# Optimization experiments

Measured on AMD Instinct MI355X. Metric: run time of the kernel, lower is better.

The kernel has to match this reference:

```python
import jax, jax.numpy as jnp
import numpy as np

E = 8        # num_adapters
K = 2        # top-k
DG = 1024    # extract_feature_size (gating input)
DI = 1024    # input_size (adapter input)
HG = 512     # gating hidden
H = 2048     # adapter hidden
C = 512      # adapter output (classes)
B = 4096     # batch
TEMP = 5.0   # gating softmax temperature
LOSS_COEF = 0.01
EPS = float(np.finfo(np.float64).eps)  # np.finfo(float).eps in combine()


def setup_inputs() -> dict:
    key = jax.random.key(0)
    ks = jax.random.split(key, 12)
    s = 0.02
    return {
        'x':   jax.random.normal(ks[0], (B, DG), jnp.float32),
        'x2':  jax.random.normal(ks[1], (B, DI), jnp.float32),
        'Wg1': jax.random.normal(ks[2], (DG, HG), jnp.float32) * s,
        'bg1': jnp.zeros((HG,), jnp.float32),
        'Wg2': jax.random.normal(ks[3], (HG, E), jnp.float32) * s,
        'bg2': jnp.zeros((E,), jnp.float32),
        'W1':  jax.random.normal(ks[4], (E, DI, H), jnp.float32) * s,
        'b1':  jnp.zeros((E, H), jnp.float32),
        'W2':  jax.random.normal(ks[5], (E, H, C), jnp.float32) * s,
        'b2':  jnp.zeros((E, C), jnp.float32),
    }


def _cv_squared(v):
    # torch .var() is unbiased (ddof=1)
    return v.var(ddof=1) / (v.mean() ** 2 + 1e-10)


def reference(x, x2, Wg1, bg1, Wg2, bg2, W1, b1, W2, b2):
    b = x.shape[0]
    # --- noisy_top_k_gating (eval path: no noise, dropout inactive) ---
    logits = jnp.maximum(x @ Wg1 + bg1, 0.0) @ Wg2 + bg2           # [B, E]
    top_vals, top_idx = jax.lax.top_k(logits, K)                   # [B, K]
    top_gates = jax.nn.softmax(top_vals / TEMP, axis=1)            # [B, K]
    gates = jnp.zeros_like(logits).at[jnp.arange(b)[:, None], top_idx].set(top_gates)  # [B, E]
    importance = gates.sum(axis=0)                                 # [E]
    load = (gates > 0).sum(axis=0).astype(jnp.float32)             # [E]
    loss = (_cv_squared(importance) + _cv_squared(load)) * LOSS_COEF
    # --- per-expert adapters (dense-equivalent of dispatch; zero gates contribute 0) ---
    h = jnp.maximum(jnp.einsum('bd,edh->ebh', x2, W1) + b1[:, None, :], 0.0)  # [E,B,H]
    out = jnp.einsum('ebh,ehc->ebc', h, W2) + b2[:, None, :]                  # [E,B,C]
    logp = jax.nn.log_softmax(out, axis=-1)                                   # adapters emit log-probs
    # --- SparseDispatcher.combine: exp -> gate-weighted sum -> eps-fill -> log ---
    combined = jnp.einsum('be,ebc->bc', gates, jnp.exp(logp))                 # [B, C]
    combined = jnp.where(combined == 0.0, EPS, combined)
    return jnp.log(combined), loss
```

## Files before the change

### kernel.cpp

```cpp
#include <hip/hip_runtime.h>
#include <hip/hip_bf16.h>
#include <math.h>

#define NE 8
#define KDG 1024
#define KDI 1024
#define NHG 512
#define NH 2048
#define NC 512
#define NB 4096

typedef float f32x4 __attribute__((ext_vector_type(4)));
typedef short s16x8 __attribute__((ext_vector_type(8)));
typedef short s16x4 __attribute__((ext_vector_type(4)));

__device__ __forceinline__ void gld_lds16(const void* g, void* l){
  __builtin_amdgcn_global_load_lds((const __attribute__((address_space(1))) void*)g,
                                   (__attribute__((address_space(3))) void*)l, 16, 0, 0);
}

__global__ void k_split_x(const float* __restrict__ in, __hip_bfloat16* __restrict__ oh,
                          __hip_bfloat16* __restrict__ ol){
  size_t i = ((size_t)blockIdx.x*256 + threadIdx.x)*4;
  f32x4 v = *reinterpret_cast<const f32x4*>(in + i);
  union { __hip_bfloat16 h[4]; s16x4 s; } uh, ul;
  #pragma unroll
  for (int j=0;j<4;j++){
    uh.h[j] = __float2bfloat16(v[j]);
    ul.h[j] = __float2bfloat16(v[j] - __bfloat162float(uh.h[j]));
  }
  *reinterpret_cast<s16x4*>(oh + i) = uh.s;
  *reinterpret_cast<s16x4*>(ol + i) = ul.s;
}

__global__ __launch_bounds__(256) void k_split_wt(const float* __restrict__ W,
                                                  __hip_bfloat16* __restrict__ Wth,
                                                  __hip_bfloat16* __restrict__ Wtl){
  __shared__ float tile[64][65];
  const int r0 = blockIdx.y*64, c0 = blockIdx.x*64;
  const int t = threadIdx.x;
  const int tx = t & 15, ty = t >> 4;
  #pragma unroll
  for (int p=0;p<4;p++){
    f32x4 v = *reinterpret_cast<const f32x4*>(&W[(size_t)(r0+ty+p*16)*NHG + c0 + tx*4]);
    #pragma unroll
    for (int j=0;j<4;j++) tile[ty+p*16][tx*4+j] = v[j];
  }
  __syncthreads();
  const int cx = t & 7, cy = t >> 3;
  #pragma unroll
  for (int p=0;p<2;p++){
    int c = cy + p*32;
    union { __hip_bfloat16 h[8]; s16x8 s; } uh, ul;
    #pragma unroll
    for (int j=0;j<8;j++){
      float v = tile[cx*8+j][c];
      uh.h[j] = __float2bfloat16(v);
      ul.h[j] = __float2bfloat16(v - __bfloat162float(uh.h[j]));
    }
    *reinterpret_cast<s16x8*>(&Wth[(size_t)(c0+c)*KDG + r0 + cx*8]) = uh.s;
    *reinterpret_cast<s16x8*>(&Wtl[(size_t)(c0+c)*KDG + r0 + cx*8]) = ul.s;
  }
}

__global__ __launch_bounds__(256) void k_gate_mm(const __hip_bfloat16* __restrict__ xh,
                                                 const __hip_bfloat16* __restrict__ xl,
                                                 const __hip_bfloat16* __restrict__ wh,
                                                 const __hip_bfloat16* __restrict__ wl,
                                                 const float* __restrict__ bg1,
                                                 float* __restrict__ hg){
  __shared__ __hip_bfloat16 Ah[2][64][32] __attribute__((aligned(16)));
  __shared__ __hip_bfloat16 Ax[2][64][32] __attribute__((aligned(16)));
  __shared__ __hip_bfloat16 Bh[2][64][32] __attribute__((aligned(16)));
  __shared__ __hip_bfloat16 Bx[2][64][32] __attribute__((aligned(16)));
  const int m0 = blockIdx.y*64, n0 = blockIdx.x*64;
  const int t = threadIdx.x, lane = t&63, wid = t>>6;
  const int rr = t>>2, kq = t&3;
  const __hip_bfloat16* pah = xh + (size_t)(m0+rr)*KDG + kq*8;
  const __hip_bfloat16* pax = xl + (size_t)(m0+rr)*KDG + kq*8;
  const __hip_bfloat16* pbh = wh + (size_t)(n0+rr)*KDG + kq*8;
  const __hip_bfloat16* pbx = wl + (size_t)(n0+rr)*KDG + kq*8;

  const int wm = wid>>1, wn = wid&1;
  f32x4 acc[2][2];
  #pragma unroll
  for (int i=0;i<2;i++)
    #pragma unroll
    for (int j=0;j<2;j++){ f32x4 z={0.f,0.f,0.f,0.f}; acc[i][j]=z; }

  auto stage = [&](int buf, int k0){
    size_t wo = (size_t)(wid<<10);
    gld_lds16(pah + k0, (char*)(&Ah[buf][0][0]) + wo);
    gld_lds16(pax + k0, (char*)(&Ax[buf][0][0]) + wo);
    gld_lds16(pbh + k0, (char*)(&Bh[buf][0][0]) + wo);
    gld_lds16(pbx + k0, (char*)(&Bx[buf][0][0]) + wo);
  };

  stage(0, 0);
  __syncthreads();
  for (int ks=0; ks<KDG/32; ++ks){
    const int buf = ks & 1;
    if (ks+1 < KDG/32) stage(buf^1, (ks+1)*32);
    const int rb = lane&15, kb = (lane>>4)*8;
    s16x8 ah[2], ax[2], bh[2], bx[2];
    #pragma unroll
    for (int mi=0;mi<2;mi++){
      ah[mi] = *reinterpret_cast<const s16x8*>(&Ah[buf][wm*32+mi*16+rb][kb]);
      ax[mi] = *reinterpret_cast<const s16x8*>(&Ax[buf][wm*32+mi*16+rb][kb]);
    }
    #pragma unroll
    for (int ni=0;ni<2;ni++){
      bh[ni] = *reinterpret_cast<const s16x8*>(&Bh[buf][wn*32+ni*16+rb][kb]);
      bx[ni] = *reinterpret_cast<const s16x8*>(&Bx[buf][wn*32+ni*16+rb][kb]);
    }
    #pragma unroll
    for (int mi=0;mi<2;mi++)
      #pragma unroll
      for (int ni=0;ni<2;ni++){
        acc[mi][ni] = __builtin_amdgcn_mfma_f32_16x16x32_bf16(ah[mi], bh[ni], acc[mi][ni], 0,0,0);
        acc[mi][ni] = __builtin_amdgcn_mfma_f32_16x16x32_bf16(ah[mi], bx[ni], acc[mi][ni], 0,0,0);
        acc[mi][ni] = __builtin_amdgcn_mfma_f32_16x16x32_bf16(ax[mi], bh[ni], acc[mi][ni], 0,0,0);
      }
    __syncthreads();
  }
  #pragma unroll
  for (int mi=0;mi<2;mi++){
    #pragma unroll
    for (int j=0;j<4;j++){
      int row = m0 + wm*32 + mi*16 + (lane>>4)*4 + j;
      #pragma unroll
      for (int ni=0;ni<2;ni++){
        int col = n0 + wn*32 + ni*16 + (lane&15);
        hg[(size_t)row*NHG + col] = fmaxf(acc[mi][ni][j] + bg1[col], 0.f);
      }
    }
  }
}

__global__ __launch_bounds__(256) void k_topk(const float* __restrict__ hg,
                                              const float* __restrict__ Wg2,
                                              const float* __restrict__ bg2,
                                              int* __restrict__ tok_e,
                                              float* __restrict__ tok_gate){
  __shared__ float w[NE][NHG];
  const int t = threadIdx.x;
  for (int i=t; i<NE*NHG; i+=256){ int k=i>>3, e=i&7; w[e][k] = Wg2[i]; }
  __syncthreads();
  const int lane = t & 63, wid = t >> 6;
  const int b = blockIdx.x*4 + wid;
  float acc[NE];
  #pragma unroll
  for (int e=0;e<NE;e++) acc[e]=0.f;
  #pragma unroll
  for (int j=0;j<8;j++){
    float hv = hg[(size_t)b*NHG + j*64 + lane];
    #pragma unroll
    for (int e=0;e<NE;e++) acc[e] += hv * w[e][j*64+lane];
  }
  #pragma unroll
  for (int e=0;e<NE;e++){
    float v = acc[e];
    #pragma unroll
    for (int s=32;s;s>>=1) v += __shfl_xor(v, s, 64);
    acc[e] = v;
  }
  if (lane==0){
    float lg[NE];
    #pragma unroll
    for (int e=0;e<NE;e++) lg[e] = acc[e] + bg2[e];
    int i1=0;
    #pragma unroll
    for (int e=1;e<NE;e++) if (lg[e] > lg[i1]) i1=e;
    int i2 = (i1==0)?1:0;
    #pragma unroll
    for (int e=0;e<NE;e++){ if (e==i1 || e==i2) continue; if (lg[e] > lg[i2]) i2=e; }
    float pr = expf((lg[i2]-lg[i1])*0.2f);
    float s  = 1.f + pr;
    tok_e[b*2]=i1;      tok_e[b*2+1]=i2;
    tok_gate[b*2]=1.f/s; tok_gate[b*2+1]=pr/s;
  }
}

__global__ __launch_bounds__(1024) void k_dispatch(const int* __restrict__ tok_e,
                                                   const float* __restrict__ tok_gate,
                                                   int* __restrict__ cnt, int* __restrict__ offs,
                                                   int* __restrict__ tlist, int* __restrict__ tok_row,
                                                   float* __restrict__ loss_out){
  __shared__ int lcnt[NE];
  __shared__ float limp[NE];
  __shared__ int loffs[NE];
  const int t = threadIdx.x;
  if (t < NE){ lcnt[t]=0; limp[t]=0.f; }
  __syncthreads();
  int e[8], p[8];
  #pragma unroll
  for (int j=0;j<8;j++){
    int i = t*8+j;
    e[j] = tok_e[i];
    p[j] = atomicAdd(&lcnt[e[j]], 1);
    atomicAdd(&limp[e[j]], tok_gate[i]);
  }
  __syncthreads();
  if (t==0){
    int o=0; float si=0.f, sl=0.f;
    for (int k=0;k<NE;k++){ loffs[k]=o; o+=lcnt[k]; si+=limp[k]; sl+=(float)lcnt[k]; }
    float mi=si/NE, ml=sl/NE, vi=0.f, vl=0.f;
    for (int k=0;k<NE;k++){ float d=limp[k]-mi; vi+=d*d; float dl=(float)lcnt[k]-ml; vl+=dl*dl; }
    vi/=(NE-1); vl/=(NE-1);
    loss_out[0] = (vi/(mi*mi+1e-10f) + vl/(ml*ml+1e-10f)) * 0.01f;
  }
  __syncthreads();
  if (t < NE){ cnt[t]=lcnt[t]; offs[t]=loffs[t]; }
  #pragma unroll
  for (int j=0;j<8;j++){
    int i = t*8+j;
    int row = loffs[e[j]] + p[j];
    tok_row[i] = row;
    tlist[row] = i>>1;
  }
}

__global__ void k_conv_x2(const float* __restrict__ in, __hip_bfloat16* __restrict__ o){
  size_t i = ((size_t)blockIdx.x*256 + threadIdx.x)*4;
  f32x4 v = *reinterpret_cast<const f32x4*>(in + i);
  union { __hip_bfloat16 h[4]; s16x4 s; } u;
  #pragma unroll
  for (int j=0;j<4;j++) u.h[j] = __float2bfloat16(v[j]);
  *reinterpret_cast<s16x4*>(o + i) = u.s;
}

template<int R, int C>
__global__ __launch_bounds__(256) void k_conv_t(const float* __restrict__ W,
                                                __hip_bfloat16* __restrict__ Wt){
  __shared__ float tile[64][65];
  const int e = blockIdx.z;
  const int r0 = blockIdx.y*64, c0 = blockIdx.x*64;
  const int t = threadIdx.x;
  const int tx = t & 15, ty = t >> 4;
  const float* src = W + (size_t)e*R*C;
  __hip_bfloat16* dst = Wt + (size_t)e*R*C;
  #pragma unroll
  for (int p=0;p<4;p++){
    f32x4 v = *reinterpret_cast<const f32x4*>(&src[(size_t)(r0+ty+p*16)*C + c0 + tx*4]);
    #pragma unroll
    for (int j=0;j<4;j++) tile[ty+p*16][tx*4+j] = v[j];
  }
  __syncthreads();
  const int cx = t & 7, cy = t >> 3;
  #pragma unroll
  for (int p=0;p<2;p++){
    int c = cy + p*32;
    union { __hip_bfloat16 h[8]; s16x8 s; } u;
    #pragma unroll
    for (int j=0;j<8;j++) u.h[j] = __float2bfloat16(tile[cx*8+j][c]);
    *reinterpret_cast<s16x8*>(&dst[(size_t)(c0+c)*R + r0 + cx*8]) = u.s;
  }
}

template<int K, int N, int BM, bool GATHER, bool RELU_OUT>
__global__ __launch_bounds__(256) void k_egemm(const __hip_bfloat16* __restrict__ Asrc,
                                               const __hip_bfloat16* __restrict__ Bt,
                                               const float* __restrict__ bias,
                                               const int* __restrict__ cnt,
                                               const int* __restrict__ offs,
                                               const int* __restrict__ tlist,
                                               void* __restrict__ Out){
  constexpr int WM = BM/64;
  constexpr int WN = 4/WM;
  constexpr int CW = 128/WN;
  constexpr int NF = CW/16;
  const int e = blockIdx.z;
  const int mcnt = cnt[e];
  const int mt = blockIdx.y;
  if (mt*BM >= mcnt) return;
  const int n0 = blockIdx.x*128;
  const int offs_e = offs[e];
  __shared__ __hip_bfloat16 Al[2][BM][32] __attribute__((aligned(16)));
  __shared__ __hip_bfloat16 Bl[2][128][32] __attribute__((aligned(16)));
  __shared__ int tk[BM];
  const int t = threadIdx.x, lane = t&63, wid = t>>6;
  for (int i=t;i<BM;i+=256){
    int m = mt*BM + i;
    int ml = m < mcnt ? m : (mcnt-1);
    tk[i] = GATHER ? tlist[offs_e + ml] : (offs_e + ml);
  }
  __syncthreads();
  const int rr = t>>2, kq = t&3;
  const __hip_bfloat16* a0 = Asrc + (size_t)tk[rr]*K + kq*8;
  const __hip_bfloat16* a1 = nullptr;
  if constexpr (BM==128) a1 = Asrc + (size_t)tk[64+rr]*K + kq*8;
  const __hip_bfloat16* Bte = Bt + ((size_t)e*N + n0)*K;
  const __hip_bfloat16* b0 = Bte + (size_t)rr*K + kq*8;
  const __hip_bfloat16* b1 = Bte + (size_t)(64+rr)*K + kq*8;

  const int wm = (WM==2) ? (wid>>1) : 0;
  const int wn = (WM==2) ? (wid&1)  : wid;
  f32x4 acc[4][NF];
  #pragma unroll
  for (int i=0;i<4;i++)
    #pragma unroll
    for (int j=0;j<NF;j++){ f32x4 z = {0.f,0.f,0.f,0.f}; acc[i][j]=z; }

  auto stage = [&](int buf, int k0){
    char* Ad = (char*)(&Al[buf][0][0]) + (wid<<10);
    char* Bd = (char*)(&Bl[buf][0][0]) + (wid<<10);
    gld_lds16(a0 + k0, Ad);
    if constexpr (BM==128) gld_lds16(a1 + k0, Ad + 4096);
    gld_lds16(b0 + k0, Bd);
    gld_lds16(b1 + k0, Bd + 4096);
  };

  stage(0, 0);
  __syncthreads();
  const int NKS = K/32;
  for (int ks=0; ks<NKS; ++ks){
    const int buf = ks & 1;
    if (ks+1 < NKS) stage(buf^1, (ks+1)*32);
    const __hip_bfloat16* Ab = &Al[buf][0][0];
    const __hip_bfloat16* Bb = &Bl[buf][0][0];
    const int rb = (lane&15), kb = (lane>>4)*8;
    s16x8 af[4], bfv[NF];
    #pragma unroll
    for (int mi=0;mi<4;mi++)
      af[mi] = *reinterpret_cast<const s16x8*>(Ab + (size_t)(wm*64 + mi*16 + rb)*32 + kb);
    #pragma unroll
    for (int ni=0;ni<NF;ni++)
      bfv[ni] = *reinterpret_cast<const s16x8*>(Bb + (size_t)(wn*CW + ni*16 + rb)*32 + kb);
    #pragma unroll
    for (int mi=0;mi<4;mi++)
      #pragma unroll
      for (int ni=0;ni<NF;ni++)
        acc[mi][ni] = __builtin_amdgcn_mfma_f32_16x16x32_bf16(af[mi], bfv[ni], acc[mi][ni], 0, 0, 0);
    __syncthreads();
  }

  const int nb = wn*CW + (lane&15);
  const int mb = wm*64 + (lane>>4)*4;
  float brg[NF];
  #pragma unroll
  for (int ni=0;ni<NF;ni++) brg[ni] = bias[e*N + n0 + nb + ni*16];
  #pragma unroll
  for (int mi=0;mi<4;mi++){
    #pragma unroll
    for (int j=0;j<4;j++){
      int m = mt*BM + mb + mi*16 + j;
      if (m < mcnt){
        size_t orow = (size_t)(offs_e + m)*N;
        #pragma unroll
        for (int ni=0;ni<NF;ni++){
          float v = acc[mi][ni][j] + brg[ni];
          if (RELU_OUT)
            ((__hip_bfloat16*)Out)[orow + n0 + nb + ni*16] = __float2bfloat16(fmaxf(v, 0.f));
          else
            ((float*)Out)[orow + n0 + nb + ni*16] = v;
        }
      }
    }
  }
}

__global__ __launch_bounds__(256) void k_combine(const float* __restrict__ outbuf,
    const int* __restrict__ tok_row, const float* __restrict__ tok_gate,
    float* __restrict__ out){
  const int t = threadIdx.x, lane = t&63, wid = t>>6;
  const int b = blockIdx.x*4 + wid;
  const float g0 = tok_gate[b*2], g1 = tok_gate[b*2+1];
  const float* r0 = outbuf + (size_t)tok_row[b*2]*NC;
  const float* r1 = outbuf + (size_t)tok_row[b*2+1]*NC;
  float v0[8], v1[8], m0=-INFINITY, m1=-INFINITY;
  #pragma unroll
  for (int i=0;i<8;i++){
    v0[i] = r0[i*64+lane]; m0 = fmaxf(m0, v0[i]);
    v1[i] = r1[i*64+lane]; m1 = fmaxf(m1, v1[i]);
  }
  #pragma unroll
  for (int s=32;s;s>>=1){ m0 = fmaxf(m0, __shfl_xor(m0,s,64)); m1 = fmaxf(m1, __shfl_xor(m1,s,64)); }
  float s0=0.f, s1=0.f;
  #pragma unroll
  for (int i=0;i<8;i++){ s0 += expf(v0[i]-m0); s1 += expf(v1[i]-m1); }
  #pragma unroll
  for (int s=32;s;s>>=1){ s0 += __shfl_xor(s0,s,64); s1 += __shfl_xor(s1,s,64); }
  const float l0 = logf(s0)+m0, l1 = logf(s1)+m1;
  #pragma unroll
  for (int i=0;i<8;i++){
    float c = g0*expf(v0[i]-l0) + g1*expf(v1[i]-l1);
    if (c == 0.f) c = 2.2204460492503131e-16f;
    out[(size_t)b*NC + i*64+lane] = logf(c);
  }
}

extern "C" void kernel_launch(void* const* d_in, const int* in_sizes, int n_in,
                              void* d_out, int out_size, void* d_ws, size_t ws_size,
                              hipStream_t stream){
  const float* x   = (const float*)d_in[0];
  const float* x2  = (const float*)d_in[1];
  const float* Wg1 = (const float*)d_in[2];
  const float* bg1 = (const float*)d_in[3];
  const float* Wg2 = (const float*)d_in[4];
  const float* bg2 = (const float*)d_in[5];
  const float* W1  = (const float*)d_in[6];
  const float* b1  = (const float*)d_in[7];
  const float* W2  = (const float*)d_in[8];
  const float* b2  = (const float*)d_in[9];
  float* out = (float*)d_out;

  char* p = (char*)d_ws;
  size_t o = 0;
  auto take = [&](size_t bytes)->char*{ char* r = p + o; o = (o + bytes + 255) & ~(size_t)255; return r; };
  int*   cnt      = (int*)  take(32);
  int*   offs     = (int*)  take(32);
  int*   tok_e    = (int*)  take((size_t)NB*2*4);
  int*   tok_row  = (int*)  take((size_t)NB*2*4);
  float* tok_gate = (float*)take((size_t)NB*2*4);
  int*   tlist    = (int*)  take((size_t)NB*2*4);
  float* hg       = (float*)take((size_t)NB*NHG*4);
  __hip_bfloat16* x2b  = (__hip_bfloat16*)take((size_t)NB*KDI*2);
  __hip_bfloat16* W1t  = (__hip_bfloat16*)take((size_t)NE*NH*KDI*2);
  __hip_bfloat16* W2t  = (__hip_bfloat16*)take((size_t)NE*NC*NH*2);
  __hip_bfloat16* hbuf = (__hip_bfloat16*)take((size_t)NB*2*NH*2);
  float* outbuf   = (float*)take((size_t)NB*2*NC*4);
  __hip_bfloat16* xh   = (__hip_bfloat16*)take((size_t)NB*KDG*2);
  __hip_bfloat16* xl   = (__hip_bfloat16*)take((size_t)NB*KDG*2);
  __hip_bfloat16* wgth = (__hip_bfloat16*)take((size_t)NHG*KDG*2);
  __hip_bfloat16* wgtl = (__hip_bfloat16*)take((size_t)NHG*KDG*2);

  k_split_x<<<dim3((NB*KDG)/(256*4)), 256, 0, stream>>>(x, xh, xl);
  k_split_wt<<<dim3(NHG/64, KDG/64), 256, 0, stream>>>(Wg1, wgth, wgtl);
  k_conv_x2<<<dim3((NB*KDI)/(256*4)), 256, 0, stream>>>(x2, x2b);
  k_conv_t<KDI, NH><<<dim3(NH/64, KDI/64, NE), 256, 0, stream>>>(W1, W1t);
  k_conv_t<NH, NC><<<dim3(NC/64, NH/64, NE), 256, 0, stream>>>(W2, W2t);
  k_gate_mm<<<dim3(NHG/64, NB/64), 256, 0, stream>>>(xh, xl, wgth, wgtl, bg1, hg);
  k_topk<<<dim3(NB/4), 256, 0, stream>>>(hg, Wg2, bg2, tok_e, tok_gate);
  k_dispatch<<<1, 1024, 0, stream>>>(tok_e, tok_gate, cnt, offs, tlist, tok_row, out + (size_t)NB*NC);
  k_egemm<KDI, NH, 128, true,  true ><<<dim3(NH/128, NB/128, NE), 256, 0, stream>>>(x2b, W1t, b1, cnt, offs, tlist, hbuf);
  k_egemm<NH,  NC, 64,  false, false><<<dim3(NC/128, NB/64, NE), 256, 0, stream>>>(hbuf, W2t, b2, cnt, offs, tlist, outbuf);
  k_combine<<<dim3(NB/4), 256, 0, stream>>>(outbuf, tok_row, tok_gate, out);
}
```

Baseline: 372.5 us.

## Pre-pack gathered x2 rows per expert and enlarge gate GEMM M tile

A new k_pack kernel replaces k_conv_x2. It gathers x2 rows in dispatch order and converts them to bf16 into a contiguous buffer, so the expert GEMMs read contiguous rows instead of using a per-block token index table. The expert GEMM drops its gather path and reads past the end of each expert's rows into padded buffers. Separately, the gate GEMM tile grows from 64x64 to 128x64, which improves reuse of the split weights and halves the block count. The cost is a gathered write of NB*2 rows instead of NB rows, plus buffer padding.

```diff
diff --git a/kernel.cpp b/kernel.cpp
--- a/kernel.cpp
+++ b/kernel.cpp
@@ -69,11 +69,11 @@
                                                  const __hip_bfloat16* __restrict__ wl,
                                                  const float* __restrict__ bg1,
                                                  float* __restrict__ hg){
-  __shared__ __hip_bfloat16 Ah[2][64][32] __attribute__((aligned(16)));
-  __shared__ __hip_bfloat16 Ax[2][64][32] __attribute__((aligned(16)));
-  __shared__ __hip_bfloat16 Bh[2][64][32] __attribute__((aligned(16)));
-  __shared__ __hip_bfloat16 Bx[2][64][32] __attribute__((aligned(16)));
-  const int m0 = blockIdx.y*64, n0 = blockIdx.x*64;
+  __shared__ __hip_bfloat16 Ah[2][128][32] __attribute__((aligned(16)));
+  __shared__ __hip_bfloat16 Ax[2][128][32] __attribute__((aligned(16)));
+  __shared__ __hip_bfloat16 Bh[2][64][32]  __attribute__((aligned(16)));
+  __shared__ __hip_bfloat16 Bx[2][64][32]  __attribute__((aligned(16)));
+  const int m0 = blockIdx.y*128, n0 = blockIdx.x*64;
   const int t = threadIdx.x, lane = t&63, wid = t>>6;
   const int rr = t>>2, kq = t&3;
   const __hip_bfloat16* pah = xh + (size_t)(m0+rr)*KDG + kq*8;
@@ -82,18 +82,20 @@
   const __hip_bfloat16* pbx = wl + (size_t)(n0+rr)*KDG + kq*8;
 
   const int wm = wid>>1, wn = wid&1;
-  f32x4 acc[2][2];
-  #pragma unroll
-  for (int i=0;i<2;i++)
+  f32x4 acc[4][2];
+  #pragma unroll
+  for (int i=0;i<4;i++)
     #pragma unroll
     for (int j=0;j<2;j++){ f32x4 z={0.f,0.f,0.f,0.f}; acc[i][j]=z; }
 
   auto stage = [&](int buf, int k0){
     size_t wo = (size_t)(wid<<10);
-    gld_lds16(pah + k0, (char*)(&Ah[buf][0][0]) + wo);
-    gld_lds16(pax + k0, (char*)(&Ax[buf][0][0]) + wo);
-    gld_lds16(pbh + k0, (char*)(&Bh[buf][0][0]) + wo);
-    gld_lds16(pbx + k0, (char*)(&Bx[buf][0][0]) + wo);
+    gld_lds16(pah + k0,            (char*)(&Ah[buf][0][0]) + wo);
+    gld_lds16(pah + 64*KDG + k0,   (char*)(&Ah[buf][0][0]) + wo + 4096);
+    gld_lds16(pax + k0,            (char*)(&Ax[buf][0][0]) + wo);
+    gld_lds16(pax + 64*KDG + k0,   (char*)(&Ax[buf][0][0]) + wo + 4096);
+    gld_lds16(pbh + k0,            (char*)(&Bh[buf][0][0]) + wo);
+    gld_lds16(pbx + k0,            (char*)(&Bx[buf][0][0]) + wo);
   };
 
   stage(0, 0);
@@ -102,11 +104,11 @@
     const int buf = ks & 1;
     if (ks+1 < KDG/32) stage(buf^1, (ks+1)*32);
     const int rb = lane&15, kb = (lane>>4)*8;
-    s16x8 ah[2], ax[2], bh[2], bx[2];
-    #pragma unroll
-    for (int mi=0;mi<2;mi++){
-      ah[mi] = *reinterpret_cast<const s16x8*>(&Ah[buf][wm*32+mi*16+rb][kb]);
-      ax[mi] = *reinterpret_cast<const s16x8*>(&Ax[buf][wm*32+mi*16+rb][kb]);
+    s16x8 ah[4], ax[4], bh[2], bx[2];
+    #pragma unroll
+    for (int mi=0;mi<4;mi++){
+      ah[mi] = *reinterpret_cast<const s16x8*>(&Ah[buf][wm*64+mi*16+rb][kb]);
+      ax[mi] = *reinterpret_cast<const s16x8*>(&Ax[buf][wm*64+mi*16+rb][kb]);
     }
     #pragma unroll
     for (int ni=0;ni<2;ni++){
@@ -114,7 +116,7 @@
       bx[ni] = *reinterpret_cast<const s16x8*>(&Bx[buf][wn*32+ni*16+rb][kb]);
     }
     #pragma unroll
-    for (int mi=0;mi<2;mi++)
+    for (int mi=0;mi<4;mi++)
       #pragma unroll
       for (int ni=0;ni<2;ni++){
         acc[mi][ni] = __builtin_amdgcn_mfma_f32_16x16x32_bf16(ah[mi], bh[ni], acc[mi][ni], 0,0,0);
@@ -123,14 +125,15 @@
       }
     __syncthreads();
   }
-  #pragma unroll
-  for (int mi=0;mi<2;mi++){
+  const int rb = lane&15;
+  #pragma unroll
+  for (int mi=0;mi<4;mi++){
     #pragma unroll
     for (int j=0;j<4;j++){
-      int row = m0 + wm*32 + mi*16 + (lane>>4)*4 + j;
+      int row = m0 + wm*64 + mi*16 + (lane>>4)*4 + j;
       #pragma unroll
       for (int ni=0;ni<2;ni++){
-        int col = n0 + wn*32 + ni*16 + (lane&15);
+        int col = n0 + wn*32 + ni*16 + rb;
         hg[(size_t)row*NHG + col] = fmaxf(acc[mi][ni][j] + bg1[col], 0.f);
       }
     }
@@ -220,13 +223,22 @@
   }
 }
 
-__global__ void k_conv_x2(const float* __restrict__ in, __hip_bfloat16* __restrict__ o){
-  size_t i = ((size_t)blockIdx.x*256 + threadIdx.x)*4;
-  f32x4 v = *reinterpret_cast<const f32x4*>(in + i);
-  union { __hip_bfloat16 h[4]; s16x4 s; } u;
-  #pragma unroll
-  for (int j=0;j<4;j++) u.h[j] = __float2bfloat16(v[j]);
-  *reinterpret_cast<s16x4*>(o + i) = u.s;
+__global__ __launch_bounds__(256) void k_pack(const float* __restrict__ x2,
+                                              const int* __restrict__ tlist,
+                                              __hip_bfloat16* __restrict__ Ap){
+  const int r = blockIdx.x*2 + (threadIdx.x>>7);
+  const int c = threadIdx.x & 127;
+  const int src = tlist[r];
+  const float* s = x2 + (size_t)src*KDI;
+  __hip_bfloat16* d = Ap + (size_t)r*KDI;
+  #pragma unroll
+  for (int p=0;p<2;p++){
+    f32x4 v = *reinterpret_cast<const f32x4*>(s + p*512 + c*4);
+    union { __hip_bfloat16 h[4]; s16x4 q; } u;
+    #pragma unroll
+    for (int j=0;j<4;j++) u.h[j] = __float2bfloat16(v[j]);
+    *reinterpret_cast<s16x4*>(d + p*512 + c*4) = u.q;
+  }
 }
 
 template<int R, int C>
@@ -257,13 +269,12 @@
   }
 }
 
-template<int K, int N, int BM, bool GATHER, bool RELU_OUT>
+template<int K, int N, int BM, bool RELU_OUT>
 __global__ __launch_bounds__(256) void k_egemm(const __hip_bfloat16* __restrict__ Asrc,
                                                const __hip_bfloat16* __restrict__ Bt,
                                                const float* __restrict__ bias,
                                                const int* __restrict__ cnt,
                                                const int* __restrict__ offs,
-                                               const int* __restrict__ tlist,
                                                void* __restrict__ Out){
   constexpr int WM = BM/64;
   constexpr int WN = 4/WM;
@@ -274,21 +285,12 @@
   const int mt = blockIdx.y;
   if (mt*BM >= mcnt) return;
   const int n0 = blockIdx.x*128;
-  const int offs_e = offs[e];
+  const int row0 = offs[e] + mt*BM;
   __shared__ __hip_bfloat16 Al[2][BM][32] __attribute__((aligned(16)));
   __shared__ __hip_bfloat16 Bl[2][128][32] __attribute__((aligned(16)));
-  __shared__ int tk[BM];
   const int t = threadIdx.x, lane = t&63, wid = t>>6;
-  for (int i=t;i<BM;i+=256){
-    int m = mt*BM + i;
-    int ml = m < mcnt ? m : (mcnt-1);
-    tk[i] = GATHER ? tlist[offs_e + ml] : (offs_e + ml);
-  }
-  __syncthreads();
   const int rr = t>>2, kq = t&3;
-  const __hip_bfloat16* a0 = Asrc + (size_t)tk[rr]*K + kq*8;
-  const __hip_bfloat16* a1 = nullptr;
-  if constexpr (BM==128) a1 = Asrc + (size_t)tk[64+rr]*K + kq*8;
+  const __hip_bfloat16* a0 = Asrc + (size_t)(row0 + rr)*K + kq*8;
   const __hip_bfloat16* Bte = Bt + ((size_t)e*N + n0)*K;
   const __hip_bfloat16* b0 = Bte + (size_t)rr*K + kq*8;
   const __hip_bfloat16* b1 = Bte + (size_t)(64+rr)*K + kq*8;
@@ -305,7 +307,7 @@
     char* Ad = (char*)(&Al[buf][0][0]) + (wid<<10);
     char* Bd = (char*)(&Bl[buf][0][0]) + (wid<<10);
     gld_lds16(a0 + k0, Ad);
-    if constexpr (BM==128) gld_lds16(a1 + k0, Ad + 4096);
+    if constexpr (BM==128) gld_lds16(a0 + (size_t)64*K + k0, Ad + 4096);
     gld_lds16(b0 + k0, Bd);
     gld_lds16(b1 + k0, Bd + 4096);
   };
@@ -345,7 +347,7 @@
     for (int j=0;j<4;j++){
       int m = mt*BM + mb + mi*16 + j;
       if (m < mcnt){
-        size_t orow = (size_t)(offs_e + m)*N;
+        size_t orow = (size_t)(row0 + mb + mi*16 + j)*N;
         #pragma unroll
         for (int ni=0;ni<NF;ni++){
           float v = acc[mi][ni][j] + brg[ni];
@@ -414,10 +416,10 @@
   float* tok_gate = (float*)take((size_t)NB*2*4);
   int*   tlist    = (int*)  take((size_t)NB*2*4);
   float* hg       = (float*)take((size_t)NB*NHG*4);
-  __hip_bfloat16* x2b  = (__hip_bfloat16*)take((size_t)NB*KDI*2);
+  __hip_bfloat16* Ap   = (__hip_bfloat16*)take((size_t)(NB*2+128)*KDI*2);
   __hip_bfloat16* W1t  = (__hip_bfloat16*)take((size_t)NE*NH*KDI*2);
   __hip_bfloat16* W2t  = (__hip_bfloat16*)take((size_t)NE*NC*NH*2);
-  __hip_bfloat16* hbuf = (__hip_bfloat16*)take((size_t)NB*2*NH*2);
+  __hip_bfloat16* hbuf = (__hip_bfloat16*)take((size_t)(NB*2+128)*NH*2);
   float* outbuf   = (float*)take((size_t)NB*2*NC*4);
   __hip_bfloat16* xh   = (__hip_bfloat16*)take((size_t)NB*KDG*2);
   __hip_bfloat16* xl   = (__hip_bfloat16*)take((size_t)NB*KDG*2);
@@ -426,13 +428,13 @@
 
   k_split_x<<<dim3((NB*KDG)/(256*4)), 256, 0, stream>>>(x, xh, xl);
   k_split_wt<<<dim3(NHG/64, KDG/64), 256, 0, stream>>>(Wg1, wgth, wgtl);
-  k_conv_x2<<<dim3((NB*KDI)/(256*4)), 256, 0, stream>>>(x2, x2b);
   k_conv_t<KDI, NH><<<dim3(NH/64, KDI/64, NE), 256, 0, stream>>>(W1, W1t);
   k_conv_t<NH, NC><<<dim3(NC/64, NH/64, NE), 256, 0, stream>>>(W2, W2t);
-  k_gate_mm<<<dim3(NHG/64, NB/64), 256, 0, stream>>>(xh, xl, wgth, wgtl, bg1, hg);
+  k_gate_mm<<<dim3(NHG/64, NB/128), 256, 0, stream>>>(xh, xl, wgth, wgtl, bg1, hg);
   k_topk<<<dim3(NB/4), 256, 0, stream>>>(hg, Wg2, bg2, tok_e, tok_gate);
   k_dispatch<<<1, 1024, 0, stream>>>(tok_e, tok_gate, cnt, offs, tlist, tok_row, out + (size_t)NB*NC);
-  k_egemm<KDI, NH, 128, true,  true ><<<dim3(NH/128, NB/128, NE), 256, 0, stream>>>(x2b, W1t, b1, cnt, offs, tlist, hbuf);
-  k_egemm<NH,  NC, 64,  false, false><<<dim3(NC/128, NB/64, NE), 256, 0, stream>>>(hbuf, W2t, b2, cnt, offs, tlist, outbuf);
+  k_pack<<<dim3(NB*2/2), 256, 0, stream>>>(x2, tlist, Ap);
+  k_egemm<KDI, NH, 128, true ><<<dim3(NH/128, NB/128, NE), 256, 0, stream>>>(Ap, W1t, b1, cnt, offs, hbuf);
+  k_egemm<NH,  NC, 64,  false><<<dim3(NC/128, NB/64, NE), 256, 0, stream>>>(hbuf, W2t, b2, cnt, offs, outbuf);
   k_combine<<<dim3(NB/4), 256, 0, stream>>>(outbuf, tok_row, tok_gate, out);
 }
```

Result: slower. 395.4 us (+6.1%).
